# Optimization experiments

Hardware: AMD Instinct MI355X
Metric: run time of the kernel (lower is better)

Reference implementation:

```python
import jax, jax.numpy as jnp
import numpy as np

WINDOWS = (5, 10, 20)
EPS = 1e-4
K_SLICES = 3
OVERLAP = 0.5


def setup_inputs() -> dict:
    key = jax.random.key(0)
    k1, k2, k3, k4 = jax.random.split(key, 4)
    B, T, H = 64, 2048, 256
    x = jax.random.normal(k1, (B, T, H), dtype=jnp.float32)
    alpha = 0.1 * jax.random.normal(k2, (H, len(WINDOWS)), dtype=jnp.float32)
    gamma = 1.0 + 0.1 * jax.random.normal(k3, (K_SLICES, H), dtype=jnp.float32)
    beta = 0.1 * jax.random.normal(k4, (K_SLICES, H), dtype=jnp.float32)
    return {"x": x, "alpha": alpha, "gamma": gamma, "beta": beta}


def _fan(x, alpha):
    # FrequencyAdaptiveNormSimple: multi-window sliding mean/std, blended by softmax(alpha).
    B, T, H = x.shape
    al = jax.nn.softmax(alpha, axis=-1)  # [H, nW]
    # prefix sums for O(T) sliding statistics (same math as unfold mean/std)
    zrow = jnp.zeros((B, 1, H), x.dtype)
    S1 = jnp.concatenate([zrow, jnp.cumsum(x, axis=1)], axis=1)        # [B, T+1, H]
    S2 = jnp.concatenate([zrow, jnp.cumsum(x * x, axis=1)], axis=1)    # [B, T+1, H]
    out = jnp.zeros_like(x)
    for wi, w in enumerate(WINDOWS):
        if w > T:
            continue
        ws = S1[:, w:, :] - S1[:, : T - w + 1, :]    # window sums, [B, T-w+1, H]
        ws2 = S2[:, w:, :] - S2[:, : T - w + 1, :]
        mu = ws / w
        var = jnp.maximum((ws2 - ws * ws / w) / (w - 1), 0.0)  # unbiased (torch std default)
        sd = jnp.maximum(jnp.sqrt(var), EPS)
        # F.pad(..., (w-1, 0), mode='replicate') on the time dim
        mu = jnp.pad(mu, ((0, 0), (w - 1, 0), (0, 0)), mode="edge")
        sd = jnp.pad(sd, ((0, 0), (w - 1, 0), (0, 0)), mode="edge")
        z = jnp.nan_to_num((x - mu) / sd, nan=0.0, posinf=0.0, neginf=0.0)
        out = out + z * al[:, wi][None, None, :]
    return out


def _san(x, gamma, beta):
    # SliceAdaptiveNormSimple: overlapping slices, per-slice (B,T) stats (detached), affine, avg.
    B, T, H = x.shape
    step = max(1, int(round(T / (K_SLICES - (K_SLICES - 1) * OVERLAP))))
    win = min(T, step + int(round(step * OVERLAP)))
    y = jnp.zeros_like(x)
    cnt = jnp.zeros((B, T, 1), x.dtype)
    s = 0
    for k in range(K_SLICES):
        e = min(T, s + win)
        if e <= s:
            break
        xk = x[:, s:e, :]
        mu = jax.lax.stop_gradient(jnp.mean(xk, axis=(0, 1), keepdims=True))
        sd = jax.lax.stop_gradient(
            jnp.maximum(jnp.std(xk, axis=(0, 1), ddof=1, keepdims=True), 1e-4)
        )
        z = jnp.nan_to_num((xk - mu) / sd, nan=0.0, posinf=0.0, neginf=0.0)
        z = z * gamma[k][None, None, :] + beta[k][None, None, :]
        y = y.at[:, s:e, :].add(z)
        cnt = cnt.at[:, s:e, :].add(1.0)
        s += step
    return y / (cnt + EPS)


def reference(x, alpha, gamma, beta):
    # StableFANSAN: out = x + SAN(FAN(x))
    return x + _san(_fan(x, alpha), gamma, beta)
```

## Files before the change

### kernel.cpp

```cpp
#include <hip/hip_runtime.h>
#include <hip/hip_fp16.h>

#define T_DIM 2048
#define H_DIM 256
#define B_DIM 64

#define FCH 64
#define FNCH (T_DIM / FCH)
#define FNCB (B_DIM * FNCH)

#define ECH 64
#define ENCH (T_DIM / ECH)
#define ENCB (B_DIM * ENCH)

#define EPS_F 1e-4f
#define R1C (1.0f / 1.0001f)
#define R2C (1.0f / 2.0001f)

#define GLB(p) ((const __attribute__((address_space(1))) void*)(p))
#define LDSP(p) ((__attribute__((address_space(3))) void*)(p))

__device__ __forceinline__ void win_stats(float s1, float s2, float inv_w, float inv_wm1,
                                          float& mu, float& isd) {
    mu = s1 * inv_w;
    float var = fmaxf((s2 - s1 * s1 * inv_w) * inv_wm1, 0.0f);
    isd = fminf(rsqrtf(var), 1e4f);
}

template <int MODE, bool FIRST>
__device__ __forceinline__ void run_main(
    float (*xs)[H_DIM], const float* __restrict__ xb, int t0, int h, int wave, int lane,
    __half2* __restrict__ s2bh, float* __restrict__ s32bh,
    float al0, float al1, float al2, float& ls1, float& ls2,
    float mu5i, float isd5i, float mu10i, float isd10i, float mu20i, float isd20i) {

    float s1_5 = 0.f, s2_5 = 0.f, s1_10 = 0.f, s2_10 = 0.f, s1_20 = 0.f, s2_20 = 0.f;

    if (!FIRST) {
#pragma unroll
        for (int j = 1; j <= 20; ++j) {
            float v = xs[(-j) & 31][h];
            s1_20 += v; s2_20 += v * v;
            if (j <= 10) { s1_10 += v; s2_10 += v * v; }
            if (j <= 5)  { s1_5  += v; s2_5  += v * v; }
        }
    }

    float fprev = 0.0f;
    for (int g = 0; g < 8; ++g) {
#pragma unroll
        for (int j = 0; j < 8; ++j) {
            const int rl = 8 * g + j;
            const int t = t0 + rl;
            const float v = xs[rl & 31][h];

            s1_5  += v; s2_5  += v * v;
            s1_10 += v; s2_10 += v * v;
            s1_20 += v; s2_20 += v * v;
            if (!FIRST || rl >= 5)  { float o = xs[(rl - 5)  & 31][h]; s1_5  -= o; s2_5  -= o * o; }
            if (!FIRST || rl >= 10) { float o = xs[(rl - 10) & 31][h]; s1_10 -= o; s2_10 -= o * o; }
            if (!FIRST || rl >= 20) { float o = xs[(rl - 20) & 31][h]; s1_20 -= o; s2_20 -= o * o; }

            float mu, isd, fan = 0.0f;
            if (!FIRST || rl >= 4)  win_stats(s1_5,  s2_5,  0.2f,  0.25f,      mu, isd);
            else { mu = mu5i;  isd = isd5i; }
            fan += (v - mu) * isd * al0;
            if (!FIRST || rl >= 9)  win_stats(s1_10, s2_10, 0.1f,  1.f / 9.f,  mu, isd);
            else { mu = mu10i; isd = isd10i; }
            fan += (v - mu) * isd * al1;
            if (!FIRST || rl >= 19) win_stats(s1_20, s2_20, 0.05f, 1.f / 19.f, mu, isd);
            else { mu = mu20i; isd = isd20i; }
            fan += (v - mu) * isd * al2;

            ls1 += fan; ls2 += fan * fan;
            if (MODE == 0) {
                if (j & 1) s2bh[(size_t)(t >> 1) * H_DIM] =
                               __halves2half2(__float2half(fprev), __float2half(fan));
                else       fprev = fan;
            } else {
                s32bh[t * H_DIM] = fan;
            }
        }
        if (g < 7) {
            __syncthreads();
            const int rl0 = 8 * g + 12 + 2 * wave;
#pragma unroll
            for (int j = 0; j < 2; ++j) {
                const int rl = rl0 + j;
                if (rl < FCH) {
                    __builtin_amdgcn_global_load_lds(
                        GLB(xb + (size_t)(t0 + rl) * H_DIM + lane * 4),
                        LDSP(&xs[rl & 31][0]), 16, 0, 0);
                }
            }
            __syncthreads();
        }
    }
}

template <int MODE>
__global__ __launch_bounds__(256)
void fan_kernel(const float* __restrict__ x, const float* __restrict__ alpha,
                float* __restrict__ part, __half* __restrict__ stash16,
                float* __restrict__ stash32) {
    __shared__ __align__(16) float xs[32][H_DIM];
    const int blk = (blockIdx.x & 7) * (FNCB / 8) + (blockIdx.x >> 3);
    const int b = blk / FNCH;
    const int c = blk % FNCH;
    const int h = threadIdx.x;
    const int wave = h >> 6;
    const int lane = h & 63;
    const int t0 = c * FCH;
    const size_t base = (size_t)b * T_DIM * H_DIM;
    const float* xb = x + base;
    __half2* s2bh = (MODE == 0)
        ? (__half2*)stash16 + (size_t)b * (T_DIM / 2) * H_DIM + h : nullptr;
    float* s32bh = (MODE == 1) ? stash32 + base + h : nullptr;

    {
        const int rl0 = -20 + 8 * wave;
#pragma unroll
        for (int j = 0; j < 8; ++j) {
            const int rl = rl0 + j;
            if (t0 + rl >= 0) {
                __builtin_amdgcn_global_load_lds(
                    GLB(xb + (size_t)(t0 + rl) * H_DIM + lane * 4),
                    LDSP(&xs[rl & 31][0]), 16, 0, 0);
            }
        }
    }

    const float a0 = alpha[h * 3 + 0], a1 = alpha[h * 3 + 1], a2 = alpha[h * 3 + 2];
    const float mx = fmaxf(a0, fmaxf(a1, a2));
    const float e0 = __expf(a0 - mx), e1 = __expf(a1 - mx), e2 = __expf(a2 - mx);
    const float einv = 1.0f / (e0 + e1 + e2);
    const float al0 = e0 * einv, al1 = e1 * einv, al2 = e2 * einv;

    float ls1 = 0.0f, ls2 = 0.0f;

    if (c == 0) {
        float mu5i, isd5i, mu10i, isd10i, mu20i, isd20i;
        float c1 = 0.f, c2 = 0.f;
#pragma unroll
        for (int j = 0; j < 20; ++j) {
            float v = xb[j * H_DIM + h];
            c1 += v; c2 += v * v;
            if (j == 4)  win_stats(c1, c2, 0.2f,  0.25f,      mu5i,  isd5i);
            if (j == 9)  win_stats(c1, c2, 0.1f,  1.f / 9.f,  mu10i, isd10i);
            if (j == 19) win_stats(c1, c2, 0.05f, 1.f / 19.f, mu20i, isd20i);
        }
        __syncthreads();
        run_main<MODE, true>(xs, xb, t0, h, wave, lane, s2bh, s32bh,
                             al0, al1, al2, ls1, ls2,
                             mu5i, isd5i, mu10i, isd10i, mu20i, isd20i);
    } else {
        __syncthreads();
        run_main<MODE, false>(xs, xb, t0, h, wave, lane, s2bh, s32bh,
                              al0, al1, al2, ls1, ls2,
                              0.f, 0.f, 0.f, 0.f, 0.f, 0.f);
    }

    part[(0 * FNCB + blk) * H_DIM + h] = ls1;
    part[(1 * FNCB + blk) * H_DIM + h] = ls2;
}

__global__ __launch_bounds__(256)
void reduce_kernel(const float* __restrict__ part, float* __restrict__ part2) {
    const int h = threadIdx.x;
    const int k = blockIdx.x >> 4;
    const int g = blockIdx.x & 15;
    float a1 = 0.f, a2 = 0.f;
    for (int i = 0; i < FNCB / 16; ++i) {
        const int blk = g * (FNCB / 16) + i;
        const int c = blk % FNCH;
        const bool member = (k == 0) ? (c < 24) : (c >= 16);
        if (member) {
            a1 += part[(0 * FNCB + blk) * H_DIM + h];
            a2 += part[(1 * FNCB + blk) * H_DIM + h];
        }
    }
    part2[((2 * k + 0) * 16 + g) * H_DIM + h] = a1;
    part2[((2 * k + 1) * 16 + g) * H_DIM + h] = a2;
}

template <bool HALF>
__global__ __launch_bounds__(256)
void epilogue_kernel(const float* __restrict__ x, const void* __restrict__ fanp,
                     const float* __restrict__ part2, const float* __restrict__ gamma,
                     const float* __restrict__ beta, float* __restrict__ out) {
    __shared__ __align__(16) float cf[4][H_DIM];
    const int tid = threadIdx.x;

    {
        float S10 = 0.f, S20 = 0.f, S11 = 0.f, S21 = 0.f;
#pragma unroll
        for (int g = 0; g < 16; ++g) {
            S10 += part2[(0 * 16 + g) * H_DIM + tid];
            S20 += part2[(1 * 16 + g) * H_DIM + tid];
            S11 += part2[(2 * 16 + g) * H_DIM + tid];
            S21 += part2[(3 * 16 + g) * H_DIM + tid];
        }
        const float N0 = 64.0f * 1536.0f, N1 = 64.0f * 1024.0f;
        float mu0 = S10 / N0;
        float v0 = fmaxf((S20 - S10 * S10 / N0) / (N0 - 1.0f), 0.0f);
        float isd0 = 1.0f / fmaxf(sqrtf(v0), EPS_F);
        float mu1 = S11 / N1;
        float v1 = fmaxf((S21 - S11 * S11 / N1) / (N1 - 1.0f), 0.0f);
        float isd1 = 1.0f / fmaxf(sqrtf(v1), EPS_F);
        float A0 = isd0 * gamma[0 * H_DIM + tid];
        float A1 = isd1 * gamma[1 * H_DIM + tid];
        cf[0][tid] = A0;
        cf[1][tid] = beta[0 * H_DIM + tid] - mu0 * A0;
        cf[2][tid] = A1;
        cf[3][tid] = beta[1 * H_DIM + tid] - mu1 * A1;
    }
    __syncthreads();

    const int blk = blockIdx.x;
    const int b = blk / ENCH;
    const int c = blk % ENCH;
    const int wave = tid >> 6;
    const int lane = tid & 63;
    const int h4 = lane * 4;

    float4 A0 = *(const float4*)&cf[0][h4];
    float4 B0 = *(const float4*)&cf[1][h4];
    float4 A1 = *(const float4*)&cf[2][h4];
    float4 B1 = *(const float4*)&cf[3][h4];
    float4 A, Bv;
    if (c < 16) {
        A  = make_float4(A0.x * R1C, A0.y * R1C, A0.z * R1C, A0.w * R1C);
        Bv = make_float4(B0.x * R1C, B0.y * R1C, B0.z * R1C, B0.w * R1C);
    } else if (c >= 24) {
        A  = make_float4(A1.x * R1C, A1.y * R1C, A1.z * R1C, A1.w * R1C);
        Bv = make_float4(B1.x * R1C, B1.y * R1C, B1.z * R1C, B1.w * R1C);
    } else {
        A  = make_float4((A0.x + A1.x) * R2C, (A0.y + A1.y) * R2C, (A0.z + A1.z) * R2C, (A0.w + A1.w) * R2C);
        Bv = make_float4((B0.x + B1.x) * R2C, (B0.y + B1.y) * R2C, (B0.z + B1.z) * R2C, (B0.w + B1.w) * R2C);
    }

    const int tbase = c * ECH + wave * 16;
    if (HALF) {
        const __half2* s2 = (const __half2*)fanp + (size_t)b * (T_DIM / 2) * H_DIM + h4;
#pragma unroll 2
        for (int p = 0; p < 8; ++p) {
            const int t = tbase + 2 * p;
            const size_t xi = ((size_t)b * T_DIM + t) * H_DIM + h4;
            float4 x0 = *(const float4*)&x[xi];
            float4 x1 = *(const float4*)&x[xi + H_DIM];
            float4 sv = *(const float4*)(s2 + (size_t)(t >> 1) * H_DIM);
            __half2 q0 = *reinterpret_cast<const __half2*>(&sv.x);
            __half2 q1 = *reinterpret_cast<const __half2*>(&sv.y);
            __half2 q2 = *reinterpret_cast<const __half2*>(&sv.z);
            __half2 q3 = *reinterpret_cast<const __half2*>(&sv.w);
            float4 o0, o1;
            o0.x = x0.x + fmaf(__low2float(q0),  A.x, Bv.x);
            o0.y = x0.y + fmaf(__low2float(q1),  A.y, Bv.y);
            o0.z = x0.z + fmaf(__low2float(q2),  A.z, Bv.z);
            o0.w = x0.w + fmaf(__low2float(q3),  A.w, Bv.w);
            o1.x = x1.x + fmaf(__high2float(q0), A.x, Bv.x);
            o1.y = x1.y + fmaf(__high2float(q1), A.y, Bv.y);
            o1.z = x1.z + fmaf(__high2float(q2), A.z, Bv.z);
            o1.w = x1.w + fmaf(__high2float(q3), A.w, Bv.w);
            *(float4*)&out[xi] = o0;
            *(float4*)&out[xi + H_DIM] = o1;
        }
    } else {
#pragma unroll 4
        for (int i = 0; i < 16; ++i) {
            const size_t idx = ((size_t)b * T_DIM + tbase + i) * H_DIM + h4;
            float4 xv = *(const float4*)&x[idx];
            float4 fv = *(const float4*)&((const float*)fanp)[idx];
            float4 o;
            o.x = xv.x + fmaf(fv.x, A.x, Bv.x);
            o.y = xv.y + fmaf(fv.y, A.y, Bv.y);
            o.z = xv.z + fmaf(fv.z, A.z, Bv.z);
            o.w = xv.w + fmaf(fv.w, A.w, Bv.w);
            *(float4*)&out[idx] = o;
        }
    }
}

extern "C" void kernel_launch(void* const* d_in, const int* in_sizes, int n_in,
                              void* d_out, int out_size, void* d_ws, size_t ws_size,
                              hipStream_t stream) {
    const float* x     = (const float*)d_in[0];
    const float* alpha = (const float*)d_in[1];
    const float* gamma = (const float*)d_in[2];
    const float* beta  = (const float*)d_in[3];
    float* out  = (float*)d_out;

    float* part  = (float*)d_ws;
    float* part2 = part + 2 * FNCB * H_DIM;
    __half* stash16 = (__half*)(part2 + 64 * H_DIM);
    const size_t need = (size_t)(2 * FNCB * H_DIM + 64 * H_DIM) * 4
                      + (size_t)B_DIM * T_DIM * H_DIM * 2;
    const bool half_path = (ws_size >= need);

    if (half_path) {
        fan_kernel<0><<<FNCB, H_DIM, 0, stream>>>(x, alpha, part, stash16, nullptr);
    } else {
        fan_kernel<1><<<FNCB, H_DIM, 0, stream>>>(x, alpha, part, nullptr, out);
    }
    reduce_kernel<<<32, H_DIM, 0, stream>>>(part, part2);
    if (half_path) {
        epilogue_kernel<true><<<ENCB, 256, 0, stream>>>(x, stash16, part2, gamma, beta, out);
    } else {
        epilogue_kernel<false><<<ENCB, 256, 0, stream>>>(x, out, part2, gamma, beta, out);
    }
}
```

Before: 343.5 us.

## Restructure FAN LDS ring into 5-group buffer with prefetch two groups ahead

```diff
diff --git a/kernel.cpp b/kernel.cpp
--- a/kernel.cpp
+++ b/kernel.cpp
@@ -29,37 +29,57 @@
 
 template <int MODE, bool FIRST>
 __device__ __forceinline__ void run_main(
-    float (*xs)[H_DIM], const float* __restrict__ xb, int t0, int h, int wave, int lane,
+    float* __restrict__ xs, const float* __restrict__ xb, int t0, int h, int wave, int lane,
     __half2* __restrict__ s2bh, float* __restrict__ s32bh,
     float al0, float al1, float al2, float& ls1, float& ls2,
     float mu5i, float isd5i, float mu10i, float isd10i, float mu20i, float isd20i) {
 
+    asm volatile("s_waitcnt vmcnt(0)" ::: "memory");
+    __builtin_amdgcn_s_barrier();
+
+    {
+        float* d = xs + (8 + 2 * wave) * H_DIM;
+        __builtin_amdgcn_global_load_lds(
+            GLB(xb + (size_t)(t0 + 8 + 2 * wave) * H_DIM + lane * 4), LDSP(d), 16, 0, 0);
+        __builtin_amdgcn_global_load_lds(
+            GLB(xb + (size_t)(t0 + 9 + 2 * wave) * H_DIM + lane * 4), LDSP(d + H_DIM), 16, 0, 0);
+    }
+
     float s1_5 = 0.f, s2_5 = 0.f, s1_10 = 0.f, s2_10 = 0.f, s1_20 = 0.f, s2_20 = 0.f;
 
     if (!FIRST) {
 #pragma unroll
         for (int j = 1; j <= 20; ++j) {
-            float v = xs[(-j) & 31][h];
+            float v = xs[(40 - j) * H_DIM + h];
             s1_20 += v; s2_20 += v * v;
             if (j <= 10) { s1_10 += v; s2_10 += v * v; }
             if (j <= 5)  { s1_5  += v; s2_5  += v * v; }
         }
     }
 
+    int gc = 0, gp1 = 4, gp2 = 3, gp3 = 2;
+
     float fprev = 0.0f;
     for (int g = 0; g < 8; ++g) {
+        const float* bc = xs + gc  * (8 * H_DIM) + h;
+        const float* b1 = xs + gp1 * (8 * H_DIM) + h;
+        const float* b2 = xs + gp2 * (8 * H_DIM) + h;
+        const float* b3 = xs + gp3 * (8 * H_DIM) + h;
 #pragma unroll
         for (int j = 0; j < 8; ++j) {
             const int rl = 8 * g + j;
             const int t = t0 + rl;
-            const float v = xs[rl & 31][h];
+            const float v = bc[j * H_DIM];
+            const float o5  = (j >= 5) ? bc[(j - 5) * H_DIM] : b1[(j + 3) * H_DIM];
+            const float o10 = (j >= 2) ? b1[(j - 2) * H_DIM] : b2[(j + 6) * H_DIM];
+            const float o20 = (j >= 4) ? b2[(j - 4) * H_DIM] : b3[(j + 4) * H_DIM];
 
             s1_5  += v; s2_5  += v * v;
             s1_10 += v; s2_10 += v * v;
             s1_20 += v; s2_20 += v * v;
-            if (!FIRST || rl >= 5)  { float o = xs[(rl - 5)  & 31][h]; s1_5  -= o; s2_5  -= o * o; }
-            if (!FIRST || rl >= 10) { float o = xs[(rl - 10) & 31][h]; s1_10 -= o; s2_10 -= o * o; }
-            if (!FIRST || rl >= 20) { float o = xs[(rl - 20) & 31][h]; s1_20 -= o; s2_20 -= o * o; }
+            if (!FIRST || rl >= 5)  { s1_5  -= o5;  s2_5  -= o5  * o5;  }
+            if (!FIRST || rl >= 10) { s1_10 -= o10; s2_10 -= o10 * o10; }
+            if (!FIRST || rl >= 20) { s1_20 -= o20; s2_20 -= o20 * o20; }
 
             float mu, isd, fan = 0.0f;
             if (!FIRST || rl >= 4)  win_stats(s1_5,  s2_5,  0.2f,  0.25f,      mu, isd);
@@ -82,18 +102,21 @@
             }
         }
         if (g < 7) {
-            __syncthreads();
-            const int rl0 = 8 * g + 12 + 2 * wave;
-#pragma unroll
-            for (int j = 0; j < 2; ++j) {
-                const int rl = rl0 + j;
-                if (rl < FCH) {
-                    __builtin_amdgcn_global_load_lds(
-                        GLB(xb + (size_t)(t0 + rl) * H_DIM + lane * 4),
-                        LDSP(&xs[rl & 31][0]), 16, 0, 0);
-                }
+            asm volatile("" ::: "memory");
+            __builtin_amdgcn_s_barrier();
+            const int rn = 8 * (g + 2) + 2 * wave;
+            if (rn < FCH) {
+                float* d = xs + (gp3 * 8 + 2 * wave) * H_DIM;
+                __builtin_amdgcn_global_load_lds(
+                    GLB(xb + (size_t)(t0 + rn) * H_DIM + lane * 4), LDSP(d), 16, 0, 0);
+                __builtin_amdgcn_global_load_lds(
+                    GLB(xb + (size_t)(t0 + rn + 1) * H_DIM + lane * 4), LDSP(d + H_DIM), 16, 0, 0);
+                asm volatile("s_waitcnt vmcnt(2)" ::: "memory");
+            } else {
+                asm volatile("s_waitcnt vmcnt(0)" ::: "memory");
             }
-            __syncthreads();
+            __builtin_amdgcn_s_barrier();
+            gp3 = gp2; gp2 = gp1; gp1 = gc; gc = (gc == 4) ? 0 : gc + 1;
         }
     }
 }
@@ -103,7 +126,7 @@
 void fan_kernel(const float* __restrict__ x, const float* __restrict__ alpha,
                 float* __restrict__ part, __half* __restrict__ stash16,
                 float* __restrict__ stash32) {
-    __shared__ __align__(16) float xs[32][H_DIM];
+    __shared__ __align__(16) float xs[40 * H_DIM];
     const int blk = (blockIdx.x & 7) * (FNCB / 8) + (blockIdx.x >> 3);
     const int b = blk / FNCH;
     const int c = blk % FNCH;
@@ -118,14 +141,15 @@
     float* s32bh = (MODE == 1) ? stash32 + base + h : nullptr;
 
     {
-        const int rl0 = -20 + 8 * wave;
-#pragma unroll
-        for (int j = 0; j < 8; ++j) {
-            const int rl = rl0 + j;
-            if (t0 + rl >= 0) {
+        const int r0 = -20 + 7 * wave;
+#pragma unroll
+        for (int j = 0; j < 7; ++j) {
+            const int r = r0 + j;
+            if (t0 + r >= 0) {
+                const int sl = (r < 0) ? r + 40 : r;
                 __builtin_amdgcn_global_load_lds(
-                    GLB(xb + (size_t)(t0 + rl) * H_DIM + lane * 4),
-                    LDSP(&xs[rl & 31][0]), 16, 0, 0);
+                    GLB(xb + (size_t)(t0 + r) * H_DIM + lane * 4),
+                    LDSP(xs + sl * H_DIM), 16, 0, 0);
             }
         }
     }
@@ -149,12 +173,10 @@
             if (j == 9)  win_stats(c1, c2, 0.1f,  1.f / 9.f,  mu10i, isd10i);
             if (j == 19) win_stats(c1, c2, 0.05f, 1.f / 19.f, mu20i, isd20i);
         }
-        __syncthreads();
         run_main<MODE, true>(xs, xb, t0, h, wave, lane, s2bh, s32bh,
                              al0, al1, al2, ls1, ls2,
                              mu5i, isd5i, mu10i, isd10i, mu20i, isd20i);
     } else {
-        __syncthreads();
         run_main<MODE, false>(xs, xb, t0, h, wave, lane, s2bh, s32bh,
                               al0, al1, al2, ls1, ls2,
                               0.f, 0.f, 0.f, 0.f, 0.f, 0.f);
```

Result: no change. 342.0 us (-0.4%).
